# Performance work log

Measured on AMD Instinct MI355X. Metric: run time of the kernel, lower is better.

## Reference

```python
import jax, jax.numpy as jnp
import numpy as np

HEADS = 8
DIM_HEAD = 64
NH = 16
NW = 16
SCALE = DIM_HEAD ** -0.5


def _avg2x2(a):
    # 2x2 average pool, stride 1, over axes 1,2 of [B,H,W,C] (== unfold+mean in torch)
    return (a[:, :-1, :-1] + a[:, 1:, :-1] + a[:, :-1, 1:] + a[:, 1:, 1:]) * 0.25


def _split_heads(t):
    B, n, _ = t.shape
    return t.reshape(B, n, HEADS, DIM_HEAD).transpose(0, 2, 1, 3)  # b h n d


def setup_inputs() -> dict:
    key = jax.random.key(0)
    ks = jax.random.split(key, 5)
    B, n, dim = 64, 482, 512
    inner = HEADS * DIM_HEAD
    return {
        "x": jax.random.normal(ks[0], (B, n, dim), jnp.float32),
        "mask": jax.random.normal(ks[1], (B, n, dim), jnp.float32),
        "W_qkv": jax.random.normal(ks[2], (3 * inner, dim), jnp.float32) * 0.02,
        "W_out": jax.random.normal(ks[3], (dim, inner), jnp.float32) * 0.02,
        "b_out": jax.random.normal(ks[4], (dim,), jnp.float32) * 0.02,
    }


def reference(x, mask, W_qkv, W_out, b_out):
    sg = jax.lax.stop_gradient
    B, n, dim = x.shape
    inner = HEADS * DIM_HEAD
    nHW = NH * NW            # 256
    nb = (NH - 1) * (NW - 1)  # 225

    # qkv projection
    qkv = x @ W_qkv.T                              # [B,n,3*inner]
    q, k, v = (
        _split_heads(t) for t in jnp.split(qkv, 3, axis=-1)
    )

    # mask path (no grad)
    mask_ = sg(mask)
    updated = (jnp.mean(mask_[:, 1:], axis=-1, keepdims=True) > 0.0).astype(x.dtype)
    updated = jnp.concatenate([jnp.ones_like(updated[:, :1]), updated], axis=1)  # [B,n,1]
    qkv_m = mask_ @ jnp.abs(sg(W_qkv)).T
    q_m, k_m, v_m = (_split_heads(t) for t in jnp.split(qkv_m, 3, axis=-1))
    q_m = q_m / (1e-6 + jnp.max(q_m, axis=2, keepdims=True))
    k_m = k_m / (1e-6 + jnp.max(k_m, axis=2, keepdims=True))
    v_m = v_m / (1e-6 + jnp.max(v_m, axis=2, keepdims=True))
    q_m, k_m, v_m = sg(q_m), sg(k_m), sg(v_m)

    # mask-modulated attention
    dots = jnp.einsum('bhnd,bhmd->bhnm', q * q_m, k * k_m) * SCALE
    attn = jax.nn.softmax(dots, axis=-1)
    out = jnp.einsum('bhnm,bhmd->bhnd', attn, v_m * v)
    out = out.transpose(0, 2, 1, 3).reshape(B, n, inner) * updated

    m = jnp.einsum('bhnm,bhmd->bhnd', sg(attn), v_m)
    m = sg(m.transpose(0, 2, 1, 3).reshape(B, n, inner) * updated)

    # overlap blending (is_overlap=True)
    inv_tail = 1.0 - updated[:, -nb:]
    inv_grid = 1.0 - updated[:, 1:nHW + 1]

    out_bridge = _avg2x2(out[:, 1:nHW + 1].reshape(B, NH, NW, inner)).reshape(B, nb, inner) * inv_tail
    out_origin = jnp.pad(out[:, -nb:].reshape(B, NH - 1, NW - 1, inner),
                         ((0, 0), (1, 1), (1, 1), (0, 0)))
    out_origin = _avg2x2(out_origin).reshape(B, nHW, inner) * inv_grid

    m_bridge = _avg2x2(m[:, 1:nHW + 1].reshape(B, NH, NW, inner)).reshape(B, nb, inner) * inv_tail
    m_origin = jnp.pad(m[:, -nb:].reshape(B, NH - 1, NW - 1, inner),
                       ((0, 0), (1, 1), (1, 1), (0, 0)))
    m_origin = _avg2x2(m_origin).reshape(B, nHW, inner) * inv_grid

    out = out.at[:, 1:nHW + 1].add(out_origin).at[:, -nb:].add(out_bridge)
    m = sg(m.at[:, 1:nHW + 1].add(m_origin).at[:, -nb:].add(m_bridge))

    # nearest-neighbor interpolation of mask means (no grad)
    mm = jnp.mean(m[:, 1:], axis=-1, keepdims=True)          # [B,n-1,1]
    a = mm[:, :nHW].reshape(B, 1, NH, NW)
    inter = jnp.repeat(jnp.repeat(a, 16, axis=2), 16, axis=3)  # [B,1,256,256]
    b = mm[:, -nb:].reshape(B, 1, NH - 1, NW - 1)
    inter_shift = jnp.repeat(jnp.repeat(b, 16, axis=2), 16, axis=3)  # [B,1,240,240]
    inter = inter.at[:, :, 8:-8, 8:-8].set((inter[:, :, 8:-8, 8:-8] + inter_shift) * 0.5)
    inter = sg(inter)

    m = sg(m @ jnp.abs(sg(W_out)).T)

    out_final = out @ W_out.T + b_out
    return out_final, m, inter
```

## Files before the change

kernel.cpp:

```cpp
#include <hip/hip_runtime.h>

#define B_      64
#define NSEQ    482
#define DIM     512
#define HEADS_  8
#define HD      64
#define QKV3    1536
#define NPAD    512
#define MROWS   (B_ * NSEQ)

typedef __bf16 v8bf __attribute__((ext_vector_type(8)));
typedef float  v4f  __attribute__((ext_vector_type(4)));
typedef unsigned int v4u __attribute__((ext_vector_type(4)));

typedef __attribute__((address_space(1))) const unsigned short gu16;
typedef __attribute__((address_space(3))) unsigned short lu16;

__device__ __forceinline__ unsigned short f2bf(float f) {
    unsigned u = __float_as_uint(f);
    u += 0x7fffu + ((u >> 16) & 1u);
    return (unsigned short)(u >> 16);
}
__device__ __forceinline__ float bf2f(unsigned short h) {
    return __uint_as_float(((unsigned)h) << 16);
}
__device__ __forceinline__ v8bf vabs8(v8bf x) {
    v4u u;
    __builtin_memcpy(&u, &x, 16);
    u &= (v4u){0x7fff7fffu, 0x7fff7fffu, 0x7fff7fffu, 0x7fff7fffu};
    v8bf r;
    __builtin_memcpy(&r, &u, 16);
    return r;
}

__global__ void k_cvt(const float* __restrict__ s, unsigned short* __restrict__ d, int n4) {
    int i = blockIdx.x * 256 + threadIdx.x;
    if (i < n4) {
        float4 v = ((const float4*)s)[i];
        ushort4 o;
        o.x = f2bf(v.x); o.y = f2bf(v.y); o.z = f2bf(v.z); o.w = f2bf(v.w);
        ((ushort4*)d)[i] = o;
    }
}

__global__ __launch_bounds__(256) void k_cvtmask(const float* __restrict__ mask,
                                                 unsigned short* __restrict__ mb,
                                                 float* __restrict__ upd) {
    int row = blockIdx.x * 4 + (threadIdx.x >> 6);
    int lane = threadIdx.x & 63;
    const float4* p = (const float4*)(mask + (size_t)row * DIM);
    ushort4* d = (ushort4*)(mb + (size_t)row * DIM);
    float s = 0.f;
    #pragma unroll
    for (int j = 0; j < 2; j++) {
        float4 v = p[j * 64 + lane];
        ushort4 o;
        o.x = f2bf(v.x); o.y = f2bf(v.y); o.z = f2bf(v.z); o.w = f2bf(v.w);
        d[j * 64 + lane] = o;
        s += v.x + v.y + v.z + v.w;
    }
    #pragma unroll
    for (int off = 32; off; off >>= 1) s += __shfl_xor(s, off);
    if (lane == 0) {
        int i = row % NSEQ;
        upd[row] = (i == 0) ? 1.f : ((s > 0.f) ? 1.f : 0.f);
    }
}

__global__ __launch_bounds__(256, 2) void k_gemm2(const unsigned short* __restrict__ A1,
                                                  const unsigned short* __restrict__ A2,
                                                  const unsigned short* __restrict__ Bw,
                                                  unsigned short* __restrict__ C1b,
                                                  unsigned short* __restrict__ C2b,
                                                  float* __restrict__ C1f,
                                                  float* __restrict__ C2f,
                                                  const float* __restrict__ bias,
                                                  int N, int K) {
    __shared__ __align__(16) unsigned short As1[128 * 32];
    __shared__ __align__(16) unsigned short As2[128 * 32];
    __shared__ __align__(16) unsigned short Bs[128 * 32];
    int tid = threadIdx.x;
    int lane = tid & 63, w = tid >> 6;
    int wm = w & 1, wn = w >> 1;
    int quad = lane >> 4, m16 = lane & 15;

    int nbx = gridDim.x, nwg = nbx * gridDim.y;
    int id = blockIdx.y * nbx + blockIdx.x;
    int q = nwg >> 3, r = nwg & 7;
    int xcd = id & 7, sub = id >> 3;
    int nid = (xcd < r ? xcd * (q + 1) : r * (q + 1) + (xcd - r) * q) + sub;
    int m0 = (nid / nbx) * 128, n0 = (nid % nbx) * 128;

    int srow = w * 16 + (lane >> 2);
    int scol = (lane & 3) * 8;
    const unsigned short* gA10 = &A1[(size_t)(m0 + srow) * K + scol];
    const unsigned short* gA11 = &A1[(size_t)(m0 + 64 + srow) * K + scol];
    const unsigned short* gA20 = &A2[(size_t)(m0 + srow) * K + scol];
    const unsigned short* gA21 = &A2[(size_t)(m0 + 64 + srow) * K + scol];
    const unsigned short* gB0  = &Bw[(size_t)(n0 + srow) * K + scol];
    const unsigned short* gB1  = &Bw[(size_t)(n0 + 64 + srow) * K + scol];
    lu16* lA10 = (lu16*)&As1[w * 512];
    lu16* lA11 = (lu16*)&As1[2048 + w * 512];
    lu16* lA20 = (lu16*)&As2[w * 512];
    lu16* lA21 = (lu16*)&As2[2048 + w * 512];
    lu16* lB0  = (lu16*)&Bs[w * 512];
    lu16* lB1  = (lu16*)&Bs[2048 + w * 512];

    v4f acc1[4][4], acc2[4][4];
    #pragma unroll
    for (int i = 0; i < 4; i++)
        #pragma unroll
        for (int j = 0; j < 4; j++) {
            acc1[i][j] = (v4f){0.f, 0.f, 0.f, 0.f};
            acc2[i][j] = (v4f){0.f, 0.f, 0.f, 0.f};
        }

    for (int k0 = 0; k0 < K; k0 += 32) {
        __builtin_amdgcn_global_load_lds((gu16*)(gA10 + k0), lA10, 16, 0, 0);
        __builtin_amdgcn_global_load_lds((gu16*)(gA11 + k0), lA11, 16, 0, 0);
        __builtin_amdgcn_global_load_lds((gu16*)(gA20 + k0), lA20, 16, 0, 0);
        __builtin_amdgcn_global_load_lds((gu16*)(gA21 + k0), lA21, 16, 0, 0);
        __builtin_amdgcn_global_load_lds((gu16*)(gB0 + k0), lB0, 16, 0, 0);
        __builtin_amdgcn_global_load_lds((gu16*)(gB1 + k0), lB1, 16, 0, 0);
        __syncthreads();
        v8bf a1[4], a2[4];
        #pragma unroll
        for (int i = 0; i < 4; i++) {
            a1[i] = *(const v8bf*)&As1[(wm * 64 + i * 16 + m16) * 32 + quad * 8];
            a2[i] = *(const v8bf*)&As2[(wm * 64 + i * 16 + m16) * 32 + quad * 8];
        }
        #pragma unroll
        for (int j = 0; j < 4; j++) {
            v8bf bb = *(const v8bf*)&Bs[(wn * 64 + j * 16 + m16) * 32 + quad * 8];
            v8bf ba = vabs8(bb);
            #pragma unroll
            for (int i = 0; i < 4; i++) {
                acc1[i][j] = __builtin_amdgcn_mfma_f32_16x16x32_bf16(a1[i], bb, acc1[i][j], 0, 0, 0);
                acc2[i][j] = __builtin_amdgcn_mfma_f32_16x16x32_bf16(a2[i], ba, acc2[i][j], 0, 0, 0);
            }
        }
        __syncthreads();
    }

    if (C1f) {
        #pragma unroll
        for (int j = 0; j < 4; j++) {
            int col = n0 + wn * 64 + j * 16 + m16;
            float bi = bias ? bias[col] : 0.f;
            #pragma unroll
            for (int i = 0; i < 4; i++) {
                int rowb = m0 + wm * 64 + i * 16 + quad * 4;
                #pragma unroll
                for (int r = 0; r < 4; r++) {
                    size_t off = (size_t)(rowb + r) * N + col;
                    C1f[off] = acc1[i][j][r] + bi;
                    C2f[off] = acc2[i][j][r];
                }
            }
        }
    } else {
        unsigned short* wbuf = &As1[w * 1024];
        int rr = lane >> 2;
        int c0 = ((lane & 3) * 2) ^ ((rr >> 1) & 7);
        size_t colb = n0 + wn * 64 + (lane & 3) * 16;
        #pragma unroll
        for (int i = 0; i < 4; i++) {
            #pragma unroll
            for (int j = 0; j < 4; j++)
                #pragma unroll
                for (int r = 0; r < 4; r++) {
                    int row = quad * 4 + r;
                    int e = j * 16 + m16;
                    int es = ((((e >> 3) ^ ((row >> 1) & 7)) << 3) | (e & 7));
                    wbuf[row * 64 + es] = f2bf(acc1[i][j][r]);
                }
            int4 p0 = *(const int4*)&wbuf[rr * 64 + c0 * 8];
            int4 p1 = *(const int4*)&wbuf[rr * 64 + (c0 ^ 1) * 8];
            size_t off0 = (size_t)(m0 + wm * 64 + i * 16 + rr) * N + colb;
            *(int4*)&C1b[off0] = p0;
            *(int4*)&C1b[off0 + 8] = p1;
        }
        #pragma unroll
        for (int i = 0; i < 4; i++) {
            #pragma unroll
            for (int j = 0; j < 4; j++)
                #pragma unroll
                for (int r = 0; r < 4; r++) {
                    int row = quad * 4 + r;
                    int e = j * 16 + m16;
                    int es = ((((e >> 3) ^ ((row >> 1) & 7)) << 3) | (e & 7));
                    wbuf[row * 64 + es] = f2bf(acc2[i][j][r]);
                }
            int4 p0 = *(const int4*)&wbuf[rr * 64 + c0 * 8];
            int4 p1 = *(const int4*)&wbuf[rr * 64 + (c0 ^ 1) * 8];
            size_t off0 = (size_t)(m0 + wm * 64 + i * 16 + rr) * N + colb;
            *(int4*)&C2b[off0] = p0;
            *(int4*)&C2b[off0 + 8] = p1;
        }
    }
}

__global__ void k_colmax(const unsigned short* __restrict__ qm, float* __restrict__ invsc) {
    int b = blockIdx.x;
    int c = blockIdx.y * 256 + threadIdx.x;
    const unsigned short* p = qm + (size_t)b * NSEQ * QKV3 + c;
    float mx = -1e30f;
    for (int i = 0; i < NSEQ; i++) mx = fmaxf(mx, bf2f(p[(size_t)i * QKV3]));
    invsc[b * QKV3 + c] = 1.f / (1e-6f + mx);
}

__global__ __launch_bounds__(256) void k_build(const unsigned short* __restrict__ qkv,
                                               const unsigned short* __restrict__ qm,
                                               const float* __restrict__ invsc,
                                               unsigned short* __restrict__ QQ,
                                               unsigned short* __restrict__ KK,
                                               unsigned short* __restrict__ VVt,
                                               unsigned short* __restrict__ VMt) {
    __shared__ unsigned short tv[64][72];
    __shared__ unsigned short tm[64][72];
    int tid = threadIdx.x;
    int dd = tid & 63, il = tid >> 6;
    int it = blockIdx.x, h = blockIdx.y, b = blockIdx.z;
    int i0 = it * 64;
    size_t bh = (size_t)(b * HEADS_ + h);
    int c = h * HD + dd;
    float invq = invsc[b * QKV3 + c] * 0.125f;
    float invk = invsc[b * QKV3 + 512 + c];
    float invv = invsc[b * QKV3 + 1024 + c];
    #pragma unroll 4
    for (int p = 0; p < 16; p++) {
        int li = p * 4 + il;
        int i = i0 + li;
        unsigned short oq = 0, ok = 0, ov = 0, om = 0;
        if (i < NSEQ) {
            size_t base = ((size_t)(b * NSEQ + i)) * QKV3 + c;
            float q  = bf2f(qkv[base]),        qv = bf2f(qm[base]);
            float kk = bf2f(qkv[base + 512]),  kv = bf2f(qm[base + 512]);
            float vv = bf2f(qkv[base + 1024]), vm = bf2f(qm[base + 1024]);
            oq = f2bf(q * qv * invq);
            ok = f2bf(kk * kv * invk);
            float vmn = vm * invv;
            ov = f2bf(vv * vmn);
            om = f2bf(vmn);
        }
        QQ[(bh * NPAD + i) * HD + dd] = oq;
        KK[(bh * NPAD + i) * HD + dd] = ok;
        tv[li][dd] = ov;
        tm[li][dd] = om;
    }
    __syncthreads();
    #pragma unroll 4
    for (int p = 0; p < 16; p++) {
        int dr = p * 4 + il;
        VVt[(bh * HD + dr) * NPAD + i0 + dd] = tv[dd][dr];
        VMt[(bh * HD + dr) * NPAD + i0 + dd] = tm[dd][dr];
    }
}

__global__ __launch_bounds__(256, 3) void k_attn(const unsigned short* __restrict__ QQ,
                                                 const unsigned short* __restrict__ KK,
                                                 const unsigned short* __restrict__ VVt,
                                                 const unsigned short* __restrict__ VMt,
                                                 const float* __restrict__ upd,
                                                 float* __restrict__ OUT1,
                                                 float* __restrict__ M1) {
    __shared__ __align__(16) unsigned short Ks[2][32 * 72];
    __shared__ __align__(16) unsigned short Vs[2][64 * 40];
    __shared__ __align__(16) unsigned short Ms[2][64 * 40];
    __shared__ __align__(16) unsigned short Ps[4][32 * 40];

    int tid = threadIdx.x;
    int w = tid >> 6, lane = tid & 63;
    int quad = lane >> 4, m16 = lane & 15;
    int id = (blockIdx.z * 8 + blockIdx.y) * 4 + blockIdx.x;
    int nid = (id & 7) * 256 + (id >> 3);
    int b = nid >> 5, h = (nid >> 2) & 7;
    int q0 = (nid & 3) * 128 + w * 32;
    size_t bh = (size_t)(b * HEADS_ + h);

    v8bf aq[2][2];
    #pragma unroll
    for (int s = 0; s < 2; s++) {
        const unsigned short* qb = &QQ[(bh * NPAD + q0 + s * 16 + m16) * HD];
        aq[s][0] = *(const v8bf*)&qb[quad * 8];
        aq[s][1] = *(const v8bf*)&qb[32 + quad * 8];
    }

    v4f vacc[2][4], macc[2][4];
    #pragma unroll
    for (int s = 0; s < 2; s++)
        #pragma unroll
        for (int dt = 0; dt < 4; dt++) {
            vacc[s][dt] = (v4f){0.f, 0.f, 0.f, 0.f};
            macc[s][dt] = (v4f){0.f, 0.f, 0.f, 0.f};
        }
    float lrun[2][4];
    #pragma unroll
    for (int s = 0; s < 2; s++)
        #pragma unroll
        for (int r = 0; r < 4; r++) lrun[s][r] = 0.f;

    const unsigned short* gK = &KK[bh * NPAD * HD + tid * 8];
    const unsigned short* gV = &VVt[(bh * HD + (tid >> 2)) * NPAD + (tid & 3) * 8];
    const unsigned short* gM = &VMt[(bh * HD + (tid >> 2)) * NPAD + (tid & 3) * 8];
    int oK = (tid >> 3) * 72 + (tid & 7) * 8;
    int oV = (tid >> 2) * 40 + (tid & 3) * 8;
    unsigned short* Pw = &Ps[w][0];

    int4 rk = *(const int4*)gK;
    int4 rv = *(const int4*)gV;
    int4 rm = *(const int4*)gM;

    for (int ic = 0; ic < 16; ++ic) {
        int buf = ic & 1;
        *(int4*)&Ks[buf][oK] = rk;
        *(int4*)&Vs[buf][oV] = rv;
        *(int4*)&Ms[buf][oV] = rm;
        if (ic < 15) {
            rk = *(const int4*)(gK + (ic + 1) * 32 * HD);
            rv = *(const int4*)(gV + (ic + 1) * 32);
            rm = *(const int4*)(gM + (ic + 1) * 32);
        }
        __syncthreads();

        v8bf kf[2][2];
        #pragma unroll
        for (int t = 0; t < 2; t++) {
            kf[t][0] = *(const v8bf*)&Ks[buf][(t * 16 + m16) * 72 + quad * 8];
            kf[t][1] = *(const v8bf*)&Ks[buf][(t * 16 + m16) * 72 + 32 + quad * 8];
        }
        v4f S[2][2];
        #pragma unroll
        for (int s = 0; s < 2; s++)
            #pragma unroll
            for (int t = 0; t < 2; t++) {
                v4f a = (v4f){0.f, 0.f, 0.f, 0.f};
                a = __builtin_amdgcn_mfma_f32_16x16x32_bf16(aq[s][0], kf[t][0], a, 0, 0, 0);
                a = __builtin_amdgcn_mfma_f32_16x16x32_bf16(aq[s][1], kf[t][1], a, 0, 0, 0);
                S[s][t] = a;
            }

        int i0 = ic * 32;
        if (i0 + 32 > NSEQ) {
            bool x0 = (i0 + m16) >= NSEQ;
            bool x1 = (i0 + 16 + m16) >= NSEQ;
            #pragma unroll
            for (int s = 0; s < 2; s++)
                #pragma unroll
                for (int r = 0; r < 4; r++) {
                    if (x0) S[s][0][r] = -1e30f;
                    if (x1) S[s][1][r] = -1e30f;
                }
        }

        #pragma unroll
        for (int s = 0; s < 2; s++)
            #pragma unroll
            for (int r = 0; r < 4; r++) {
                float e0 = __expf(S[s][0][r]);
                float e1 = __expf(S[s][1][r]);
                lrun[s][r] += e0 + e1;
                Pw[(s * 16 + quad * 4 + r) * 40 + m16] = f2bf(e0);
                Pw[(s * 16 + quad * 4 + r) * 40 + 16 + m16] = f2bf(e1);
            }

        v8bf ap[2];
        ap[0] = *(const v8bf*)&Pw[m16 * 40 + quad * 8];
        ap[1] = *(const v8bf*)&Pw[(16 + m16) * 40 + quad * 8];

        #pragma unroll
        for (int dt = 0; dt < 4; dt++) {
            v8bf bv = *(const v8bf*)&Vs[buf][(dt * 16 + m16) * 40 + quad * 8];
            v8bf bm = *(const v8bf*)&Ms[buf][(dt * 16 + m16) * 40 + quad * 8];
            #pragma unroll
            for (int s = 0; s < 2; s++) {
                vacc[s][dt] = __builtin_amdgcn_mfma_f32_16x16x32_bf16(ap[s], bv, vacc[s][dt], 0, 0, 0);
                macc[s][dt] = __builtin_amdgcn_mfma_f32_16x16x32_bf16(ap[s], bm, macc[s][dt], 0, 0, 0);
            }
        }
    }

    #pragma unroll
    for (int s = 0; s < 2; s++)
        #pragma unroll
        for (int r = 0; r < 4; r++) {
            float sum = lrun[s][r];
            sum += __shfl_xor(sum, 1);
            sum += __shfl_xor(sum, 2);
            sum += __shfl_xor(sum, 4);
            sum += __shfl_xor(sum, 8);
            float iv = 1.f / sum;
            int iq = q0 + s * 16 + quad * 4 + r;
            if (iq < NSEQ) {
                float u = upd[b * NSEQ + iq] * iv;
                size_t off = ((size_t)(b * NSEQ + iq)) * DIM + h * HD + m16;
                #pragma unroll
                for (int dt = 0; dt < 4; dt++) {
                    OUT1[off + dt * 16] = vacc[s][dt][r] * u;
                    M1[off + dt * 16]   = macc[s][dt][r] * u;
                }
            }
        }
}

__global__ __launch_bounds__(256) void k_blend(const float* __restrict__ O1,
                                               const float* __restrict__ Mm,
                                               const float* __restrict__ upd,
                                               unsigned short* __restrict__ O2,
                                               unsigned short* __restrict__ M2,
                                               float* __restrict__ mm) {
    int blk = blockIdx.x;
    int b = blk / NSEQ, i = blk - b * NSEQ;
    int tid = threadIdx.x;
    size_t rb = (size_t)blk * DIM;
    int ns = 0;
    size_t src[4];
    float wgt = 0.f;
    if (i >= 1) {
        wgt = 0.25f * (1.f - upd[blk]);
        if (wgt != 0.f) {
            if (i <= 256) {
                int g = i - 1, gy = g >> 4, gx = g & 15;
                #pragma unroll
                for (int dy = 0; dy < 2; dy++)
                    #pragma unroll
                    for (int dx = 0; dx < 2; dx++) {
                        int sy = gy - 1 + dy, sx = gx - 1 + dx;
                        if (sy >= 0 && sy < 15 && sx >= 0 && sx < 15)
                            src[ns++] = ((size_t)(b * NSEQ + 257 + sy * 15 + sx)) * DIM;
                    }
            } else {
                int t = i - 257, ty = t / 15, tx = t - ty * 15;
                #pragma unroll
                for (int dy = 0; dy < 2; dy++)
                    #pragma unroll
                    for (int dx = 0; dx < 2; dx++)
                        src[ns++] = ((size_t)(b * NSEQ + 1 + (ty + dy) * 16 + (tx + dx))) * DIM;
            }
        }
    }
    float msum = 0.f;
    for (int c = tid; c < DIM; c += 256) {
        float o = O1[rb + c], m = Mm[rb + c];
        float ao = 0.f, am = 0.f;
        for (int s = 0; s < ns; s++) { ao += O1[src[s] + c]; am += Mm[src[s] + c]; }
        o += wgt * ao;
        m += wgt * am;
        O2[rb + c] = f2bf(o);
        M2[rb + c] = f2bf(m);
        msum += m;
    }
    #pragma unroll
    for (int off = 32; off; off >>= 1) msum += __shfl_xor(msum, off);
    __shared__ float red[4];
    if ((tid & 63) == 0) red[tid >> 6] = msum;
    __syncthreads();
    if (tid == 0 && i >= 1)
        mm[b * 481 + i - 1] = (red[0] + red[1] + red[2] + red[3]) * (1.f / 512.f);
}

__global__ void k_inter(const float* __restrict__ mm, float* __restrict__ dst) {
    int idx = blockIdx.x * 256 + threadIdx.x;
    int b = idx >> 16, rem = idx & 65535;
    int y = rem >> 8, x = rem & 255;
    const float* mb = mm + b * 481;
    float v = mb[((y >> 4) << 4) + (x >> 4)];
    if (y >= 8 && y < 248 && x >= 8 && x < 248)
        v = 0.5f * (v + mb[256 + ((y - 8) >> 4) * 15 + ((x - 8) >> 4)]);
    dst[idx] = v;
}

extern "C" void kernel_launch(void* const* d_in, const int* in_sizes, int n_in,
                              void* d_out, int out_size, void* d_ws, size_t ws_size,
                              hipStream_t stream) {
    const float* x    = (const float*)d_in[0];
    const float* mask = (const float*)d_in[1];
    const float* Wqkv = (const float*)d_in[2];
    const float* Wout = (const float*)d_in[3];
    const float* bout = (const float*)d_in[4];
    float* out = (float*)d_out;

    char* ws = (char*)d_ws;
    size_t o = 0;
    auto alloc = [&](size_t bytes) -> char* {
        char* r = ws + o;
        o += (bytes + 255) & ~(size_t)255;
        return r;
    };
    unsigned short* xb    = (unsigned short*)alloc((size_t)MROWS * DIM * 2);
    unsigned short* maskb = (unsigned short*)alloc((size_t)MROWS * DIM * 2);
    unsigned short* Wb    = (unsigned short*)alloc((size_t)QKV3 * DIM * 2);
    unsigned short* Wob   = (unsigned short*)alloc((size_t)DIM * DIM * 2);
    unsigned short* qkvb  = (unsigned short*)alloc((size_t)MROWS * QKV3 * 2);
    unsigned short* qkvmb = (unsigned short*)alloc((size_t)MROWS * QKV3 * 2);
    float* upd  = (float*)alloc((size_t)MROWS * 4);
    float* invs = (float*)alloc((size_t)B_ * QKV3 * 4);
    float* mm   = (float*)alloc((size_t)B_ * 481 * 4);
    unsigned short* QQ  = (unsigned short*)alloc((size_t)B_ * HEADS_ * NPAD * HD * 2);
    unsigned short* KK  = (unsigned short*)alloc((size_t)B_ * HEADS_ * NPAD * HD * 2);
    unsigned short* VVt = (unsigned short*)alloc((size_t)B_ * HEADS_ * NPAD * HD * 2);
    unsigned short* VMt = (unsigned short*)alloc((size_t)B_ * HEADS_ * NPAD * HD * 2);
    float* OUT1 = (float*)qkvb;
    float* M1p  = (float*)qkvmb;
    unsigned short* O2 = xb;
    unsigned short* M2 = maskb;

    k_cvt<<<(MROWS * DIM / 4) / 256, 256, 0, stream>>>(x, xb, MROWS * DIM / 4);
    k_cvtmask<<<MROWS / 4, 256, 0, stream>>>(mask, maskb, upd);
    k_cvt<<<(QKV3 * DIM / 4) / 256, 256, 0, stream>>>(Wqkv, Wb, QKV3 * DIM / 4);
    k_cvt<<<(DIM * DIM / 4) / 256, 256, 0, stream>>>(Wout, Wob, DIM * DIM / 4);

    dim3 g1(QKV3 / 128, MROWS / 128);
    k_gemm2<<<g1, 256, 0, stream>>>(xb, maskb, Wb, qkvb, qkvmb,
                                    nullptr, nullptr, nullptr, QKV3, DIM);

    k_colmax<<<dim3(B_, QKV3 / 256), 256, 0, stream>>>(qkvmb, invs);
    k_build<<<dim3(8, HEADS_, B_), 256, 0, stream>>>(qkvb, qkvmb, invs, QQ, KK, VVt, VMt);

    k_attn<<<dim3(4, HEADS_, B_), 256, 0, stream>>>(QQ, KK, VVt, VMt, upd, OUT1, M1p);

    k_blend<<<MROWS, 256, 0, stream>>>(OUT1, M1p, upd, O2, M2, mm);
    k_inter<<<(B_ * 65536) / 256, 256, 0, stream>>>(mm, out + (size_t)2 * MROWS * DIM);

    dim3 g2(DIM / 128, MROWS / 128);
    k_gemm2<<<g2, 256, 0, stream>>>(O2, M2, Wob, nullptr, nullptr,
                                    out, out + (size_t)MROWS * DIM, bout, DIM, DIM);
}
```

Measured before the change: 760.5 us.

## Double-buffer LDS tiles in the fused dual GEMM to overlap loads with MFMA

```diff
diff --git a/kernel.cpp b/kernel.cpp
--- a/kernel.cpp
+++ b/kernel.cpp
@@ -76,9 +76,9 @@
                                                   float* __restrict__ C2f,
                                                   const float* __restrict__ bias,
                                                   int N, int K) {
-    __shared__ __align__(16) unsigned short As1[128 * 32];
-    __shared__ __align__(16) unsigned short As2[128 * 32];
-    __shared__ __align__(16) unsigned short Bs[128 * 32];
+    __shared__ __align__(16) unsigned short As1[2][128 * 32];
+    __shared__ __align__(16) unsigned short As2[2][128 * 32];
+    __shared__ __align__(16) unsigned short Bs[2][128 * 32];
     int tid = threadIdx.x;
     int lane = tid & 63, w = tid >> 6;
     int wm = w & 1, wn = w >> 1;
@@ -99,12 +99,12 @@
     const unsigned short* gA21 = &A2[(size_t)(m0 + 64 + srow) * K + scol];
     const unsigned short* gB0  = &Bw[(size_t)(n0 + srow) * K + scol];
     const unsigned short* gB1  = &Bw[(size_t)(n0 + 64 + srow) * K + scol];
-    lu16* lA10 = (lu16*)&As1[w * 512];
-    lu16* lA11 = (lu16*)&As1[2048 + w * 512];
-    lu16* lA20 = (lu16*)&As2[w * 512];
-    lu16* lA21 = (lu16*)&As2[2048 + w * 512];
-    lu16* lB0  = (lu16*)&Bs[w * 512];
-    lu16* lB1  = (lu16*)&Bs[2048 + w * 512];
+    lu16* lA10 = (lu16*)&As1[0][w * 512];
+    lu16* lA11 = (lu16*)&As1[0][2048 + w * 512];
+    lu16* lA20 = (lu16*)&As2[0][w * 512];
+    lu16* lA21 = (lu16*)&As2[0][2048 + w * 512];
+    lu16* lB0  = (lu16*)&Bs[0][w * 512];
+    lu16* lB1  = (lu16*)&Bs[0][2048 + w * 512];
 
     v4f acc1[4][4], acc2[4][4];
     #pragma unroll
@@ -115,31 +115,44 @@
             acc2[i][j] = (v4f){0.f, 0.f, 0.f, 0.f};
         }
 
-    for (int k0 = 0; k0 < K; k0 += 32) {
-        __builtin_amdgcn_global_load_lds((gu16*)(gA10 + k0), lA10, 16, 0, 0);
-        __builtin_amdgcn_global_load_lds((gu16*)(gA11 + k0), lA11, 16, 0, 0);
-        __builtin_amdgcn_global_load_lds((gu16*)(gA20 + k0), lA20, 16, 0, 0);
-        __builtin_amdgcn_global_load_lds((gu16*)(gA21 + k0), lA21, 16, 0, 0);
-        __builtin_amdgcn_global_load_lds((gu16*)(gB0 + k0), lB0, 16, 0, 0);
-        __builtin_amdgcn_global_load_lds((gu16*)(gB1 + k0), lB1, 16, 0, 0);
+    auto STAGE = [&](int bb, int s) {
+        int ko = s << 5;
+        int bo = bb << 12;
+        __builtin_amdgcn_global_load_lds((gu16*)(gA10 + ko), lA10 + bo, 16, 0, 0);
+        __builtin_amdgcn_global_load_lds((gu16*)(gA11 + ko), lA11 + bo, 16, 0, 0);
+        __builtin_amdgcn_global_load_lds((gu16*)(gA20 + ko), lA20 + bo, 16, 0, 0);
+        __builtin_amdgcn_global_load_lds((gu16*)(gA21 + ko), lA21 + bo, 16, 0, 0);
+        __builtin_amdgcn_global_load_lds((gu16*)(gB0  + ko), lB0  + bo, 16, 0, 0);
+        __builtin_amdgcn_global_load_lds((gu16*)(gB1  + ko), lB1  + bo, 16, 0, 0);
+    };
+    auto COMPUTE = [&](int bb) {
+        v8bf a1[4], a2[4];
+        #pragma unroll
+        for (int i = 0; i < 4; i++) {
+            a1[i] = *(const v8bf*)&As1[bb][(wm * 64 + i * 16 + m16) * 32 + quad * 8];
+            a2[i] = *(const v8bf*)&As2[bb][(wm * 64 + i * 16 + m16) * 32 + quad * 8];
+        }
+        #pragma unroll
+        for (int j = 0; j < 4; j++) {
+            v8bf bf = *(const v8bf*)&Bs[bb][(wn * 64 + j * 16 + m16) * 32 + quad * 8];
+            v8bf ba = vabs8(bf);
+            #pragma unroll
+            for (int i = 0; i < 4; i++) {
+                acc1[i][j] = __builtin_amdgcn_mfma_f32_16x16x32_bf16(a1[i], bf, acc1[i][j], 0, 0, 0);
+                acc2[i][j] = __builtin_amdgcn_mfma_f32_16x16x32_bf16(a2[i], ba, acc2[i][j], 0, 0, 0);
+            }
+        }
+    };
+
+    int steps = K >> 5;
+    STAGE(0, 0);
+    for (int s = 0; s < steps; s += 2) {
         __syncthreads();
-        v8bf a1[4], a2[4];
-        #pragma unroll
-        for (int i = 0; i < 4; i++) {
-            a1[i] = *(const v8bf*)&As1[(wm * 64 + i * 16 + m16) * 32 + quad * 8];
-            a2[i] = *(const v8bf*)&As2[(wm * 64 + i * 16 + m16) * 32 + quad * 8];
-        }
-        #pragma unroll
-        for (int j = 0; j < 4; j++) {
-            v8bf bb = *(const v8bf*)&Bs[(wn * 64 + j * 16 + m16) * 32 + quad * 8];
-            v8bf ba = vabs8(bb);
-            #pragma unroll
-            for (int i = 0; i < 4; i++) {
-                acc1[i][j] = __builtin_amdgcn_mfma_f32_16x16x32_bf16(a1[i], bb, acc1[i][j], 0, 0, 0);
-                acc2[i][j] = __builtin_amdgcn_mfma_f32_16x16x32_bf16(a2[i], ba, acc2[i][j], 0, 0, 0);
-            }
-        }
+        STAGE(1, s + 1);
+        COMPUTE(0);
         __syncthreads();
+        if (s + 2 < steps) STAGE(0, s + 2);
+        COMPUTE(1);
     }
 
     if (C1f) {
@@ -159,7 +172,7 @@
             }
         }
     } else {
-        unsigned short* wbuf = &As1[w * 1024];
+        unsigned short* wbuf = &As1[0][w * 1024];
         int rr = lane >> 2;
         int c0 = ((lane & 3) * 2) ^ ((rr >> 1) & 7);
         size_t colb = n0 + wn * 64 + (lane & 3) * 16;
```

Result: no change. 756.4 us (-0.5%).
